# Kernel tuning notes

Hardware: AMD Instinct MI355X
Metric: run time of the kernel (lower is better)

Reference implementation:

```python
import jax, jax.numpy as jnp
import numpy as np

STATE_DIM = 28224  # 84*84*4 flattened Atari stack
N_EPISODE = 8192
FEATURE_DIM = 32
K_NEAREST = 10
C = 0.001
EPS_KERNEL = 0.001


def setup_inputs() -> dict:
    key = jax.random.key(0)
    ks = jax.random.split(key, 5)
    s = jax.random.normal(ks[0], (1, STATE_DIM), dtype=jnp.float32)
    episode = jax.random.normal(ks[1], (N_EPISODE, STATE_DIM), dtype=jnp.float32)
    dm2 = jnp.ones((1,), dtype=jnp.float32)  # running distance stat (torch inits 0.0; 1.0 avoids div-by-zero)
    # fan-in scaled weights so activations stay O(1)
    W1 = jax.random.normal(ks[2], (STATE_DIM, 128), dtype=jnp.float32) / np.sqrt(STATE_DIM)
    b1 = jnp.zeros((128,), dtype=jnp.float32)
    W2 = jax.random.normal(ks[3], (128, 64), dtype=jnp.float32) / np.sqrt(128.0)
    b2 = jnp.zeros((64,), dtype=jnp.float32)
    W3 = jax.random.normal(ks[4], (64, FEATURE_DIM), dtype=jnp.float32) / np.sqrt(64.0)
    b3 = jnp.zeros((FEATURE_DIM,), dtype=jnp.float32)
    return {"s": s, "episode": episode, "dm2": dm2,
            "W1": W1, "b1": b1, "W2": W2, "b2": b2, "W3": W3, "b3": b3}


def _embed(x, W1, b1, W2, b2, W3, b3):
    h = jax.nn.relu(x @ W1 + b1)
    h = jax.nn.relu(h @ W2 + b2)
    return h @ W3 + b3  # [*, FEATURE_DIM]


def reference(s, episode, dm2, W1, b1, W2, b2, W3, b3):
    z_s = _embed(s, W1, b1, W2, b2, W3, b3)          # [1, F]
    z_ep = _embed(episode, W1, b1, W2, b2, W3, b3)   # [N, F]
    dist = jnp.linalg.norm(z_s - z_ep, axis=1)       # [N]
    kernel = EPS_KERNEL / (dist / dm2[0] + EPS_KERNEL)
    top_k_kernel, _ = jax.lax.top_k(kernel, K_NEAREST)           # largest kernel values
    neg_top_dist, _ = jax.lax.top_k(-dist, K_NEAREST)            # smallest distances
    top_k_dist = -neg_top_dist
    new_dm2 = 0.99 * dm2[0] + 0.01 * jnp.mean(top_k_dist)        # running-stat update
    reward_episodic = 1.0 / (jnp.sqrt(jnp.mean(top_k_kernel)) + C)
    return reward_episodic, new_dm2
```

## Files before the change

### kernel.cpp

```cpp
#include <hip/hip_runtime.h>
#include <hip/hip_bf16.h>

typedef __attribute__((ext_vector_type(8))) __bf16 bf16x8;
typedef __attribute__((ext_vector_type(4))) float f32x4;
typedef __attribute__((ext_vector_type(4))) unsigned short u16x4;

#define STATE_DIM 28224
#define NEP 8192
#define MPAD 8320
#define KSPLIT 7
#define KSTEPS 63
#define BK 64
#define EPSK 0.001f
#define CC 0.001f

#define WT_BYTES   (441 * 8192 * 2)
#define PART_BYTES (KSPLIT * MPAD * 128 * 4)
#define Z_BYTES    (MPAD * 32 * 4)
#define DIST_BYTES (NEP * 4)
#define WS_NEEDED  (WT_BYTES + PART_BYTES + Z_BYTES + DIST_BYTES)

__device__ __forceinline__ unsigned short f2bf(float f) {
    unsigned int u = __float_as_uint(f);
    u += 0x7fffu + ((u >> 16) & 1u);
    return (unsigned short)(u >> 16);
}

__device__ __forceinline__ void glds16(const void* g, void* l) {
    __builtin_amdgcn_global_load_lds(
        (const __attribute__((address_space(1))) unsigned int*)g,
        (__attribute__((address_space(3))) unsigned int*)l, 16, 0, 0);
}

__global__ __launch_bounds__(256) void prep_wt(const float* __restrict__ W1,
                                               unsigned short* __restrict__ WtS) {
    __shared__ __align__(16) unsigned short img[8192];
    const int c = blockIdx.x;
    const int tid = threadIdx.x;
    const int k0 = c * 64;
#pragma unroll
    for (int i = 0; i < 32; ++i) {
        const int f = i * 256 + tid;
        const int k = f >> 7, n = f & 127;
        const float wv = W1[(size_t)(k0 + k) * 128 + n];
        const int ad = ((n * 128 + k * 2) ^ ((n & 7) << 4)) >> 1;
        img[ad] = f2bf(wv);
    }
    __syncthreads();
    unsigned short* dst = WtS + (size_t)c * 8192;
#pragma unroll
    for (int i = 0; i < 4; ++i) {
        const int f = i * 256 + tid;
        *reinterpret_cast<uint4*>(dst + f * 8) =
            *reinterpret_cast<const uint4*>(img + f * 8);
    }
}

__global__ __launch_bounds__(256, 2) void gemm1(const float* __restrict__ ep,
                                                const float* __restrict__ s,
                                                const unsigned short* __restrict__ WtS,
                                                float* __restrict__ part) {
    __shared__ __align__(16) unsigned char smA[128 * 64 * 2];
    __shared__ __align__(16) unsigned char smB[2][128 * 64 * 2];

    const int bid = blockIdx.x;
    const int ks = bid / 65;
    const int mt = bid % 65;
    const int tid = threadIdx.x;
    const int kBase = ks * (KSTEPS * BK);
    const int chunkBase = ks * KSTEPS;

    const int mBase = tid >> 4;
    const int kOff = (tid & 15) * 4;
    const int swzW = (mBase & 7) << 4;

    const bool last = (mt == 64);
    const int rowBase = mt * 128;

    float4 aR[8];

    auto loadA = [&](int kc) {
#pragma unroll
        for (int i = 0; i < 8; ++i) {
            const int m = mBase + i * 16;
            const int rg = rowBase + m;
            if (!last) {
                aR[i] = *reinterpret_cast<const float4*>(ep + (size_t)rg * STATE_DIM + kc + kOff);
            } else {
                if (rg < NEP)
                    aR[i] = *reinterpret_cast<const float4*>(ep + (size_t)rg * STATE_DIM + kc + kOff);
                else if (rg == NEP)
                    aR[i] = *reinterpret_cast<const float4*>(s + kc + kOff);
                else
                    aR[i] = make_float4(0.f, 0.f, 0.f, 0.f);
            }
        }
    };

    const int w = tid >> 6;
    const int lane = tid & 63;

    auto stageB = [&](int chunkIdx, int buf) {
        const char* cb = (const char*)(WtS + (size_t)chunkIdx * 8192);
#pragma unroll
        for (int r2 = 0; r2 < 4; ++r2) {
            const int off = ((r2 << 2) + w) << 10;
            glds16(cb + off + (lane << 4), &smB[buf][off]);
        }
    };

    auto writeLdsA = [&]() {
#pragma unroll
        for (int i = 0; i < 8; ++i) {
            const int m = mBase + i * 16;
            u16x4 av;
            av[0] = f2bf(aR[i].x); av[1] = f2bf(aR[i].y);
            av[2] = f2bf(aR[i].z); av[3] = f2bf(aR[i].w);
            const int ad = (m * 128 + kOff * 2) ^ swzW;
            *reinterpret_cast<u16x4*>(smA + ad) = av;
        }
    };

    const int wr = w >> 1, wc = w & 1;
    const int l15 = lane & 15, lq = lane >> 4;
    const int swzF = (l15 & 7) << 4;

    f32x4 acc[4][4] = {};

    auto compute = [&](int buf) {
#pragma unroll
        for (int kh = 0; kh < 2; ++kh) {
            bf16x8 af[4], bf[4];
#pragma unroll
            for (int mf = 0; mf < 4; ++mf) {
                const int row = wr * 64 + mf * 16 + l15;
                const int ad = (row * 128 + (kh * 32 + lq * 8) * 2) ^ swzF;
                af[mf] = *reinterpret_cast<const bf16x8*>(smA + ad);
            }
#pragma unroll
            for (int nf = 0; nf < 4; ++nf) {
                const int row = wc * 64 + nf * 16 + l15;
                const int ad = (row * 128 + (kh * 32 + lq * 8) * 2) ^ swzF;
                bf[nf] = *reinterpret_cast<const bf16x8*>(smB[buf] + ad);
            }
#pragma unroll
            for (int mf = 0; mf < 4; ++mf)
#pragma unroll
                for (int nf = 0; nf < 4; ++nf)
                    acc[mf][nf] = __builtin_amdgcn_mfma_f32_16x16x32_bf16(
                        af[mf], bf[nf], acc[mf][nf], 0, 0, 0);
        }
    };

    loadA(kBase);
    stageB(chunkBase, 0);
    int buf = 0;
    for (int t2 = 0; t2 < KSTEPS; ++t2) {
        __syncthreads();
        writeLdsA();
        __syncthreads();
        if (t2 + 1 < KSTEPS) {
            loadA(kBase + (t2 + 1) * BK);
            stageB(chunkBase + t2 + 1, buf ^ 1);
        }
        compute(buf);
        buf ^= 1;
    }

    float* po = part + ((size_t)ks * MPAD + rowBase) * 128;
#pragma unroll
    for (int mf = 0; mf < 4; ++mf)
#pragma unroll
        for (int nf = 0; nf < 4; ++nf)
#pragma unroll
            for (int v = 0; v < 4; ++v) {
                const int row = wr * 64 + mf * 16 + lq * 4 + v;
                const int col = wc * 64 + nf * 16 + l15;
                po[(size_t)row * 128 + col] = acc[mf][nf][v];
            }
}

__global__ __launch_bounds__(256) void mlp23(const float* __restrict__ part,
                                             const float* __restrict__ b1,
                                             const float* __restrict__ W2,
                                             const float* __restrict__ b2,
                                             const float* __restrict__ W3,
                                             const float* __restrict__ b3,
                                             float* __restrict__ z) {
    __shared__ float W2t[64 * 129];
    __shared__ float W3t[32 * 65];
    __shared__ float b1L[128], b2L[64], b3L[32];
    __shared__ float h1buf[4][128];
    __shared__ float h2buf[4][64];

    const int tid = threadIdx.x;
#pragma unroll
    for (int i = 0; i < 32; ++i) {
        int f = tid + i * 256;
        W2t[(f & 63) * 129 + (f >> 6)] = W2[f];
    }
#pragma unroll
    for (int i = 0; i < 8; ++i) {
        int f = tid + i * 256;
        W3t[(f & 31) * 65 + (f >> 5)] = W3[f];
    }
    if (tid < 128) b1L[tid] = b1[tid];
    if (tid < 64) b2L[tid] = b2[tid];
    if (tid < 32) b3L[tid] = b3[tid];
    __syncthreads();

    const int w = tid >> 6, l = tid & 63;
    const int base = blockIdx.x * 16 + w * 4;
    for (int rr = 0; rr < 4; ++rr) {
        const int r = base + rr;
        if (r > NEP) continue;
        float h1a = b1L[l], h1b = b1L[l + 64];
#pragma unroll
        for (int p = 0; p < KSPLIT; ++p) {
            const float* pp = part + ((size_t)p * MPAD + r) * 128;
            h1a += pp[l];
            h1b += pp[l + 64];
        }
        h1a = fmaxf(h1a, 0.f);
        h1b = fmaxf(h1b, 0.f);
        h1buf[w][l] = h1a;
        h1buf[w][l + 64] = h1b;
        float a2 = b2L[l];
#pragma unroll 8
        for (int k = 0; k < 128; ++k) a2 += h1buf[w][k] * W2t[l * 129 + k];
        a2 = fmaxf(a2, 0.f);
        h2buf[w][l] = a2;
        const int c = l & 31;
        float a3 = b3L[c];
#pragma unroll 8
        for (int k = 0; k < 64; ++k) a3 += h2buf[w][k] * W3t[c * 65 + k];
        if (l < 32) z[(size_t)r * 32 + c] = a3;
    }
}

__global__ __launch_bounds__(256) void dist_k(const float* __restrict__ z,
                                              float* __restrict__ dist) {
    __shared__ float zs[32];
    const int t = threadIdx.x;
    if (t < 32) zs[t] = z[(size_t)NEP * 32 + t];
    __syncthreads();
    const int r = blockIdx.x * 256 + t;
    const float* zr = z + (size_t)r * 32;
    float d2 = 0.f;
#pragma unroll
    for (int c2 = 0; c2 < 32; ++c2) {
        const float d = zr[c2] - zs[c2];
        d2 += d * d;
    }
    dist[r] = sqrtf(d2);
}

__global__ __launch_bounds__(256) void top10_k(const float* __restrict__ dist,
                                               const float* __restrict__ dm2,
                                               float* __restrict__ out) {
    const int t = threadIdx.x;
    float v[32];
#pragma unroll
    for (int i = 0; i < 32; ++i) v[i] = dist[i * 256 + t];

    __shared__ float wv[4];
    __shared__ int wi[4];

    const float dm = dm2[0];
    float sd = 0.f, sk = 0.f;

    for (int round = 0; round < 10; ++round) {
        float bv = 3.0e38f;
        int bi = 0x7fffffff;
#pragma unroll
        for (int i = 0; i < 32; ++i) {
            const float x = v[i];
            const int idx = i * 256 + t;
            if (x < bv) { bv = x; bi = idx; }
        }
#pragma unroll
        for (int sft = 1; sft < 64; sft <<= 1) {
            const float ov = __shfl_xor(bv, sft);
            const int oi = __shfl_xor(bi, sft);
            if (ov < bv || (ov == bv && oi < bi)) { bv = ov; bi = oi; }
        }
        const int wid = t >> 6;
        if ((t & 63) == 0) { wv[wid] = bv; wi[wid] = bi; }
        __syncthreads();
        bv = wv[0]; bi = wi[0];
#pragma unroll
        for (int k = 1; k < 4; ++k) {
            const float ov = wv[k]; const int oi = wi[k];
            if (ov < bv || (ov == bv && oi < bi)) { bv = ov; bi = oi; }
        }
        __syncthreads();
#pragma unroll
        for (int i = 0; i < 32; ++i)
            if (bi == i * 256 + t) v[i] = 3.0e38f;
        sd += bv;
        sk += EPSK / (bv / dm + EPSK);
    }

    if (t == 0) {
        const float meand = sd * 0.1f;
        const float meank = sk * 0.1f;
        out[0] = 1.0f / (sqrtf(meank) + CC);
        out[1] = 0.99f * dm + 0.01f * meand;
    }
}

extern "C" void kernel_launch(void* const* d_in, const int* in_sizes, int n_in,
                              void* d_out, int out_size, void* d_ws, size_t ws_size,
                              hipStream_t stream) {
    const float* s   = (const float*)d_in[0];
    const float* ep  = (const float*)d_in[1];
    const float* dm2 = (const float*)d_in[2];
    const float* W1  = (const float*)d_in[3];
    const float* b1  = (const float*)d_in[4];
    const float* W2  = (const float*)d_in[5];
    const float* b2  = (const float*)d_in[6];
    const float* W3  = (const float*)d_in[7];
    const float* b3  = (const float*)d_in[8];
    float* out = (float*)d_out;

    if (ws_size < (size_t)WS_NEEDED) return;

    unsigned short* WtS = (unsigned short*)d_ws;
    float* part = (float*)((char*)d_ws + WT_BYTES);
    float* zbuf = (float*)((char*)d_ws + WT_BYTES + PART_BYTES);
    float* dist = (float*)((char*)d_ws + WT_BYTES + PART_BYTES + Z_BYTES);

    hipLaunchKernelGGL(prep_wt, dim3(441), dim3(256), 0, stream, W1, WtS);
    hipLaunchKernelGGL(gemm1, dim3(65 * KSPLIT), dim3(256), 0, stream, ep, s, WtS, part);
    hipLaunchKernelGGL(mlp23, dim3(520), dim3(256), 0, stream, part, b1, W2, b2, W3, b3, zbuf);
    hipLaunchKernelGGL(dist_k, dim3(32), dim3(256), 0, stream, zbuf, dist);
    hipLaunchKernelGGL(top10_k, dim3(1), dim3(256), 0, stream, dist, dm2, out);
}
```

Baseline: 228.5 us.

## Halve GEMM1 M-tile to 64 rows for more blocks and split MLP dot-product chains

The first-layer GEMM now uses 64-row M tiles instead of 128. That raises the grid from 455 to 903 blocks and shrinks per-block LDS and accumulator registers, so three blocks can fit per CU. Each thread now loads 4 contiguous float4 per row, and each wave covers all 64 rows across 32 output columns. The intent is better occupancy and CU coverage for what is a memory-bound streaming of the 924MB episode matrix. Separately, the layer-2/3 dot products in mlp23 use several independent accumulators to break serial FMA dependencies, at the cost of a changed floating-point summation order.

Result: slower. 273.2 us (+19.5%).

```diff
diff --git a/kernel.cpp b/kernel.cpp
--- a/kernel.cpp
+++ b/kernel.cpp
@@ -7,7 +7,8 @@
 
 #define STATE_DIM 28224
 #define NEP 8192
-#define MPAD 8320
+#define NMT 129
+#define MPAD 8256
 #define KSPLIT 7
 #define KSTEPS 63
 #define BK 64
@@ -56,45 +57,46 @@
     }
 }
 
-__global__ __launch_bounds__(256, 2) void gemm1(const float* __restrict__ ep,
+__global__ __launch_bounds__(256, 3) void gemm1(const float* __restrict__ ep,
                                                 const float* __restrict__ s,
                                                 const unsigned short* __restrict__ WtS,
                                                 float* __restrict__ part) {
-    __shared__ __align__(16) unsigned char smA[128 * 64 * 2];
+    __shared__ __align__(16) unsigned char smA[64 * 64 * 2];
     __shared__ __align__(16) unsigned char smB[2][128 * 64 * 2];
 
     const int bid = blockIdx.x;
-    const int ks = bid / 65;
-    const int mt = bid % 65;
+    const int ks = bid / NMT;
+    const int mt = bid % NMT;
     const int tid = threadIdx.x;
     const int kBase = ks * (KSTEPS * BK);
     const int chunkBase = ks * KSTEPS;
 
-    const int mBase = tid >> 4;
-    const int kOff = (tid & 15) * 4;
-    const int swzW = (mBase & 7) << 4;
-
-    const bool last = (mt == 64);
-    const int rowBase = mt * 128;
-
-    float4 aR[8];
+    const int mRow = tid >> 2;
+    const int kSeg = (tid & 3) * 16;
+    const int swzW = (mRow & 7) << 4;
+
+    const bool last = (mt == NMT - 1);
+    const int rowBase = mt * 64;
+
+    float4 aR[4];
 
     auto loadA = [&](int kc) {
-#pragma unroll
-        for (int i = 0; i < 8; ++i) {
-            const int m = mBase + i * 16;
-            const int rg = rowBase + m;
-            if (!last) {
-                aR[i] = *reinterpret_cast<const float4*>(ep + (size_t)rg * STATE_DIM + kc + kOff);
-            } else {
-                if (rg < NEP)
-                    aR[i] = *reinterpret_cast<const float4*>(ep + (size_t)rg * STATE_DIM + kc + kOff);
-                else if (rg == NEP)
-                    aR[i] = *reinterpret_cast<const float4*>(s + kc + kOff);
-                else
-                    aR[i] = make_float4(0.f, 0.f, 0.f, 0.f);
-            }
-        }
+        const int rg = rowBase + mRow;
+        const float* src;
+        if (!last) {
+            src = ep + (size_t)rg * STATE_DIM + kc + kSeg;
+        } else if (rg < NEP) {
+            src = ep + (size_t)rg * STATE_DIM + kc + kSeg;
+        } else if (rg == NEP) {
+            src = s + kc + kSeg;
+        } else {
+#pragma unroll
+            for (int j = 0; j < 4; ++j) aR[j] = make_float4(0.f, 0.f, 0.f, 0.f);
+            return;
+        }
+#pragma unroll
+        for (int j = 0; j < 4; ++j)
+            aR[j] = *reinterpret_cast<const float4*>(src + j * 4);
     };
 
     const int w = tid >> 6;
@@ -111,42 +113,40 @@
 
     auto writeLdsA = [&]() {
 #pragma unroll
-        for (int i = 0; i < 8; ++i) {
-            const int m = mBase + i * 16;
+        for (int j = 0; j < 4; ++j) {
             u16x4 av;
-            av[0] = f2bf(aR[i].x); av[1] = f2bf(aR[i].y);
-            av[2] = f2bf(aR[i].z); av[3] = f2bf(aR[i].w);
-            const int ad = (m * 128 + kOff * 2) ^ swzW;
+            av[0] = f2bf(aR[j].x); av[1] = f2bf(aR[j].y);
+            av[2] = f2bf(aR[j].z); av[3] = f2bf(aR[j].w);
+            const int ad = (mRow * 128 + (kSeg + j * 4) * 2) ^ swzW;
             *reinterpret_cast<u16x4*>(smA + ad) = av;
         }
     };
 
-    const int wr = w >> 1, wc = w & 1;
     const int l15 = lane & 15, lq = lane >> 4;
     const int swzF = (l15 & 7) << 4;
 
-    f32x4 acc[4][4] = {};
+    f32x4 acc[4][2] = {};
 
     auto compute = [&](int buf) {
 #pragma unroll
         for (int kh = 0; kh < 2; ++kh) {
-            bf16x8 af[4], bf[4];
+            bf16x8 af[4], bf[2];
 #pragma unroll
             for (int mf = 0; mf < 4; ++mf) {
-                const int row = wr * 64 + mf * 16 + l15;
+                const int row = mf * 16 + l15;
                 const int ad = (row * 128 + (kh * 32 + lq * 8) * 2) ^ swzF;
                 af[mf] = *reinterpret_cast<const bf16x8*>(smA + ad);
             }
 #pragma unroll
-            for (int nf = 0; nf < 4; ++nf) {
-                const int row = wc * 64 + nf * 16 + l15;
+            for (int nf = 0; nf < 2; ++nf) {
+                const int row = w * 32 + nf * 16 + l15;
                 const int ad = (row * 128 + (kh * 32 + lq * 8) * 2) ^ swzF;
                 bf[nf] = *reinterpret_cast<const bf16x8*>(smB[buf] + ad);
             }
 #pragma unroll
             for (int mf = 0; mf < 4; ++mf)
 #pragma unroll
-                for (int nf = 0; nf < 4; ++nf)
+                for (int nf = 0; nf < 2; ++nf)
                     acc[mf][nf] = __builtin_amdgcn_mfma_f32_16x16x32_bf16(
                         af[mf], bf[nf], acc[mf][nf], 0, 0, 0);
         }
@@ -171,11 +171,11 @@
 #pragma unroll
     for (int mf = 0; mf < 4; ++mf)
 #pragma unroll
-        for (int nf = 0; nf < 4; ++nf)
+        for (int nf = 0; nf < 2; ++nf)
 #pragma unroll
             for (int v = 0; v < 4; ++v) {
-                const int row = wr * 64 + mf * 16 + lq * 4 + v;
-                const int col = wc * 64 + nf * 16 + l15;
+                const int row = mf * 16 + lq * 4 + v;
+                const int col = w * 32 + nf * 16 + l15;
                 po[(size_t)row * 128 + col] = acc[mf][nf][v];
             }
 }
@@ -225,16 +225,28 @@
         h1b = fmaxf(h1b, 0.f);
         h1buf[w][l] = h1a;
         h1buf[w][l + 64] = h1b;
-        float a2 = b2L[l];
+        float s0 = 0.f, s1 = 0.f, s2 = 0.f, s3 = 0.f;
+        const float* wr2 = &W2t[l * 129];
+        const float* hb = h1buf[w];
 #pragma unroll 8
-        for (int k = 0; k < 128; ++k) a2 += h1buf[w][k] * W2t[l * 129 + k];
-        a2 = fmaxf(a2, 0.f);
+        for (int k = 0; k < 32; ++k) {
+            s0 += hb[k]      * wr2[k];
+            s1 += hb[k + 32] * wr2[k + 32];
+            s2 += hb[k + 64] * wr2[k + 64];
+            s3 += hb[k + 96] * wr2[k + 96];
+        }
+        float a2 = fmaxf(b2L[l] + ((s0 + s1) + (s2 + s3)), 0.f);
         h2buf[w][l] = a2;
         const int c = l & 31;
-        float a3 = b3L[c];
+        const float* wr3 = &W3t[c * 65];
+        const float* h2 = h2buf[w];
+        float t0 = 0.f, t1 = 0.f;
 #pragma unroll 8
-        for (int k = 0; k < 64; ++k) a3 += h2buf[w][k] * W3t[c * 65 + k];
-        if (l < 32) z[(size_t)r * 32 + c] = a3;
+        for (int k = 0; k < 32; ++k) {
+            t0 += h2[k]      * wr3[k];
+            t1 += h2[k + 32] * wr3[k + 32];
+        }
+        if (l < 32) z[(size_t)r * 32 + c] = b3L[c] + t0 + t1;
     }
 }
 
@@ -331,8 +343,8 @@
     float* dist = (float*)((char*)d_ws + WT_BYTES + PART_BYTES + Z_BYTES);
 
     hipLaunchKernelGGL(prep_wt, dim3(441), dim3(256), 0, stream, W1, WtS);
-    hipLaunchKernelGGL(gemm1, dim3(65 * KSPLIT), dim3(256), 0, stream, ep, s, WtS, part);
-    hipLaunchKernelGGL(mlp23, dim3(520), dim3(256), 0, stream, part, b1, W2, b2, W3, b3, zbuf);
+    hipLaunchKernelGGL(gemm1, dim3(NMT * KSPLIT), dim3(256), 0, stream, ep, s, WtS, part);
+    hipLaunchKernelGGL(mlp23, dim3(MPAD / 16), dim3(256), 0, stream, part, b1, W2, b2, W3, b3, zbuf);
     hipLaunchKernelGGL(dist_k, dim3(32), dim3(256), 0, stream, zbuf, dist);
     hipLaunchKernelGGL(top10_k, dim3(1), dim3(256), 0, stream, dist, dm2, out);
 }
```

## Load GEMM operands directly into registers, dropping LDS staging and block barriers

Applied to the files above, without the earlier changes.

The first-layer GEMM no longer stages A and B tiles through shared memory. Each lane now loads its MFMA fragments straight from global memory into registers, using double-buffered register sets and an occasional s_barrier to keep waves loosely in step. W1 is pre-transposed into a plain row-major [128 x STATE_DIM] bf16 layout to suit this. The last M-tile reuses the s row and writes only row 0. The mlp23 dot products are split into several independent partial sums. The change removes LDS traffic and __syncthreads, but each fragment load is a strided 32-byte access per lane, so global coalescing and cache reuse across waves may suffer.

Result: slower. 413.1 us (+80.8%).

```diff
diff --git a/kernel.cpp b/kernel.cpp
--- a/kernel.cpp
+++ b/kernel.cpp
@@ -3,18 +3,17 @@
 
 typedef __attribute__((ext_vector_type(8))) __bf16 bf16x8;
 typedef __attribute__((ext_vector_type(4))) float f32x4;
-typedef __attribute__((ext_vector_type(4))) unsigned short u16x4;
 
 #define STATE_DIM 28224
 #define NEP 8192
 #define MPAD 8320
 #define KSPLIT 7
-#define KSTEPS 63
-#define BK 64
+#define KRANGE 4032
+#define KSTEPS 126
 #define EPSK 0.001f
 #define CC 0.001f
 
-#define WT_BYTES   (441 * 8192 * 2)
+#define WT_BYTES   (128 * 28224 * 2)
 #define PART_BYTES (KSPLIT * MPAD * 128 * 4)
 #define Z_BYTES    (MPAD * 32 * 4)
 #define DIST_BYTES (NEP * 4)
@@ -26,148 +25,100 @@
     return (unsigned short)(u >> 16);
 }
 
-__device__ __forceinline__ void glds16(const void* g, void* l) {
-    __builtin_amdgcn_global_load_lds(
-        (const __attribute__((address_space(1))) unsigned int*)g,
-        (__attribute__((address_space(3))) unsigned int*)l, 16, 0, 0);
-}
-
 __global__ __launch_bounds__(256) void prep_wt(const float* __restrict__ W1,
-                                               unsigned short* __restrict__ WtS) {
-    __shared__ __align__(16) unsigned short img[8192];
-    const int c = blockIdx.x;
-    const int tid = threadIdx.x;
-    const int k0 = c * 64;
-#pragma unroll
-    for (int i = 0; i < 32; ++i) {
-        const int f = i * 256 + tid;
-        const int k = f >> 7, n = f & 127;
-        const float wv = W1[(size_t)(k0 + k) * 128 + n];
-        const int ad = ((n * 128 + k * 2) ^ ((n & 7) << 4)) >> 1;
-        img[ad] = f2bf(wv);
+                                               unsigned short* __restrict__ Wt) {
+    __shared__ float tile[32 * 65];
+    const int b = blockIdx.x;
+    const int kt = b % 441, nt = b / 441;
+    const int k0 = kt * 64, n0 = nt * 32;
+    const int t = threadIdx.x;
+#pragma unroll
+    for (int i = 0; i < 8; ++i) {
+        int f = t + i * 256;
+        int kk = f >> 5, nn = f & 31;
+        tile[nn * 65 + kk] = W1[(size_t)(k0 + kk) * 128 + n0 + nn];
     }
     __syncthreads();
-    unsigned short* dst = WtS + (size_t)c * 8192;
-#pragma unroll
-    for (int i = 0; i < 4; ++i) {
-        const int f = i * 256 + tid;
-        *reinterpret_cast<uint4*>(dst + f * 8) =
-            *reinterpret_cast<const uint4*>(img + f * 8);
+#pragma unroll
+    for (int i = 0; i < 8; ++i) {
+        int f = t + i * 256;
+        int nn = f >> 6, kk = f & 63;
+        Wt[(size_t)(n0 + nn) * STATE_DIM + k0 + kk] = f2bf(tile[nn * 65 + kk]);
     }
 }
 
 __global__ __launch_bounds__(256, 2) void gemm1(const float* __restrict__ ep,
                                                 const float* __restrict__ s,
-                                                const unsigned short* __restrict__ WtS,
+                                                const unsigned short* __restrict__ Wt,
                                                 float* __restrict__ part) {
-    __shared__ __align__(16) unsigned char smA[128 * 64 * 2];
-    __shared__ __align__(16) unsigned char smB[2][128 * 64 * 2];
-
     const int bid = blockIdx.x;
     const int ks = bid / 65;
     const int mt = bid % 65;
     const int tid = threadIdx.x;
-    const int kBase = ks * (KSTEPS * BK);
-    const int chunkBase = ks * KSTEPS;
-
-    const int mBase = tid >> 4;
-    const int kOff = (tid & 15) * 4;
-    const int swzW = (mBase & 7) << 4;
-
-    const bool last = (mt == 64);
-    const int rowBase = mt * 128;
-
-    float4 aR[8];
-
-    auto loadA = [&](int kc) {
-#pragma unroll
-        for (int i = 0; i < 8; ++i) {
-            const int m = mBase + i * 16;
-            const int rg = rowBase + m;
-            if (!last) {
-                aR[i] = *reinterpret_cast<const float4*>(ep + (size_t)rg * STATE_DIM + kc + kOff);
-            } else {
-                if (rg < NEP)
-                    aR[i] = *reinterpret_cast<const float4*>(ep + (size_t)rg * STATE_DIM + kc + kOff);
-                else if (rg == NEP)
-                    aR[i] = *reinterpret_cast<const float4*>(s + kc + kOff);
-                else
-                    aR[i] = make_float4(0.f, 0.f, 0.f, 0.f);
-            }
-        }
-    };
-
-    const int w = tid >> 6;
-    const int lane = tid & 63;
-
-    auto stageB = [&](int chunkIdx, int buf) {
-        const char* cb = (const char*)(WtS + (size_t)chunkIdx * 8192);
-#pragma unroll
-        for (int r2 = 0; r2 < 4; ++r2) {
-            const int off = ((r2 << 2) + w) << 10;
-            glds16(cb + off + (lane << 4), &smB[buf][off]);
-        }
-    };
-
-    auto writeLdsA = [&]() {
-#pragma unroll
-        for (int i = 0; i < 8; ++i) {
-            const int m = mBase + i * 16;
-            u16x4 av;
-            av[0] = f2bf(aR[i].x); av[1] = f2bf(aR[i].y);
-            av[2] = f2bf(aR[i].z); av[3] = f2bf(aR[i].w);
-            const int ad = (m * 128 + kOff * 2) ^ swzW;
-            *reinterpret_cast<u16x4*>(smA + ad) = av;
-        }
-    };
-
+    const int w = tid >> 6, lane = tid & 63;
     const int wr = w >> 1, wc = w & 1;
     const int l15 = lane & 15, lq = lane >> 4;
-    const int swzF = (l15 & 7) << 4;
+    const int kBase = ks * KRANGE;
+    const bool last = (mt == 64);
+
+    const float* aP[4];
+    const unsigned short* bP[4];
+#pragma unroll
+    for (int mf = 0; mf < 4; ++mf) {
+        const int row = mt * 128 + wr * 64 + mf * 16 + l15;
+        aP[mf] = last ? (s + kBase + lq * 8)
+                      : (ep + (size_t)row * STATE_DIM + kBase + lq * 8);
+    }
+#pragma unroll
+    for (int nf = 0; nf < 4; ++nf) {
+        const int n = wc * 64 + nf * 16 + l15;
+        bP[nf] = Wt + (size_t)n * STATE_DIM + kBase + lq * 8;
+    }
 
     f32x4 acc[4][4] = {};
 
-    auto compute = [&](int buf) {
-#pragma unroll
-        for (int kh = 0; kh < 2; ++kh) {
-            bf16x8 af[4], bf[4];
-#pragma unroll
-            for (int mf = 0; mf < 4; ++mf) {
-                const int row = wr * 64 + mf * 16 + l15;
-                const int ad = (row * 128 + (kh * 32 + lq * 8) * 2) ^ swzF;
-                af[mf] = *reinterpret_cast<const bf16x8*>(smA + ad);
-            }
-#pragma unroll
-            for (int nf = 0; nf < 4; ++nf) {
-                const int row = wc * 64 + nf * 16 + l15;
-                const int ad = (row * 128 + (kh * 32 + lq * 8) * 2) ^ swzF;
-                bf[nf] = *reinterpret_cast<const bf16x8*>(smB[buf] + ad);
-            }
-#pragma unroll
-            for (int mf = 0; mf < 4; ++mf)
-#pragma unroll
-                for (int nf = 0; nf < 4; ++nf)
-                    acc[mf][nf] = __builtin_amdgcn_mfma_f32_16x16x32_bf16(
-                        af[mf], bf[nf], acc[mf][nf], 0, 0, 0);
-        }
-    };
-
-    loadA(kBase);
-    stageB(chunkBase, 0);
-    int buf = 0;
-    for (int t2 = 0; t2 < KSTEPS; ++t2) {
-        __syncthreads();
-        writeLdsA();
-        __syncthreads();
-        if (t2 + 1 < KSTEPS) {
-            loadA(kBase + (t2 + 1) * BK);
-            stageB(chunkBase + t2 + 1, buf ^ 1);
-        }
-        compute(buf);
-        buf ^= 1;
-    }
-
-    float* po = part + ((size_t)ks * MPAD + rowBase) * 128;
+    float4 a0A[4], a1A[4], a0B[4], a1B[4];
+    uint4 bA[4], bB[4];
+
+#define LOADS(A0, A1, BB, t2)                                                   \
+    {                                                                           \
+        const int ko = (t2) * 32;                                               \
+        _Pragma("unroll") for (int mf = 0; mf < 4; ++mf) {                      \
+            A0[mf] = *reinterpret_cast<const float4*>(aP[mf] + ko);             \
+            A1[mf] = *reinterpret_cast<const float4*>(aP[mf] + ko + 4);         \
+        }                                                                       \
+        _Pragma("unroll") for (int nf = 0; nf < 4; ++nf)                        \
+            BB[nf] = *reinterpret_cast<const uint4*>(bP[nf] + ko);              \
+    }
+
+#define COMPUTE(A0, A1, BB)                                                     \
+    {                                                                           \
+        bf16x8 af[4];                                                           \
+        _Pragma("unroll") for (int mf = 0; mf < 4; ++mf) {                      \
+            af[mf][0] = (__bf16)A0[mf].x; af[mf][1] = (__bf16)A0[mf].y;         \
+            af[mf][2] = (__bf16)A0[mf].z; af[mf][3] = (__bf16)A0[mf].w;         \
+            af[mf][4] = (__bf16)A1[mf].x; af[mf][5] = (__bf16)A1[mf].y;         \
+            af[mf][6] = (__bf16)A1[mf].z; af[mf][7] = (__bf16)A1[mf].w;         \
+        }                                                                       \
+        _Pragma("unroll") for (int mf = 0; mf < 4; ++mf)                        \
+            _Pragma("unroll") for (int nf = 0; nf < 4; ++nf)                    \
+                acc[mf][nf] = __builtin_amdgcn_mfma_f32_16x16x32_bf16(          \
+                    af[mf], *reinterpret_cast<const bf16x8*>(&BB[nf]),          \
+                    acc[mf][nf], 0, 0, 0);                                      \
+    }
+
+    LOADS(a0A, a1A, bA, 0);
+    for (int t2 = 0; t2 < KSTEPS; t2 += 2) {
+        LOADS(a0B, a1B, bB, t2 + 1);
+        COMPUTE(a0A, a1A, bA);
+        if (t2 + 2 < KSTEPS) LOADS(a0A, a1A, bA, t2 + 2);
+        COMPUTE(a0B, a1B, bB);
+        if ((t2 & 15) == 14) __builtin_amdgcn_s_barrier();
+    }
+#undef LOADS
+#undef COMPUTE
+
+    float* po = part + ((size_t)ks * MPAD + mt * 128) * 128;
 #pragma unroll
     for (int mf = 0; mf < 4; ++mf)
 #pragma unroll
@@ -176,7 +127,8 @@
             for (int v = 0; v < 4; ++v) {
                 const int row = wr * 64 + mf * 16 + lq * 4 + v;
                 const int col = wc * 64 + nf * 16 + l15;
-                po[(size_t)row * 128 + col] = acc[mf][nf][v];
+                if (!last || row == 0)
+                    po[(size_t)row * 128 + col] = acc[mf][nf][v];
             }
 }
 
@@ -225,16 +177,28 @@
         h1b = fmaxf(h1b, 0.f);
         h1buf[w][l] = h1a;
         h1buf[w][l + 64] = h1b;
-        float a2 = b2L[l];
+        float s0 = 0.f, s1 = 0.f, s2 = 0.f, s3 = 0.f;
+        const float* wr2 = &W2t[l * 129];
+        const float* hb = h1buf[w];
 #pragma unroll 8
-        for (int k = 0; k < 128; ++k) a2 += h1buf[w][k] * W2t[l * 129 + k];
-        a2 = fmaxf(a2, 0.f);
+        for (int k = 0; k < 32; ++k) {
+            s0 += hb[k]      * wr2[k];
+            s1 += hb[k + 32] * wr2[k + 32];
+            s2 += hb[k + 64] * wr2[k + 64];
+            s3 += hb[k + 96] * wr2[k + 96];
+        }
+        float a2 = fmaxf(b2L[l] + ((s0 + s1) + (s2 + s3)), 0.f);
         h2buf[w][l] = a2;
         const int c = l & 31;
-        float a3 = b3L[c];
+        const float* wr3 = &W3t[c * 65];
+        const float* h2 = h2buf[w];
+        float t0 = 0.f, t1 = 0.f;
 #pragma unroll 8
-        for (int k = 0; k < 64; ++k) a3 += h2buf[w][k] * W3t[c * 65 + k];
-        if (l < 32) z[(size_t)r * 32 + c] = a3;
+        for (int k = 0; k < 32; ++k) {
+            t0 += h2[k]      * wr3[k];
+            t1 += h2[k + 32] * wr3[k + 32];
+        }
+        if (l < 32) z[(size_t)r * 32 + c] = b3L[c] + t0 + t1;
     }
 }
 
@@ -325,14 +289,14 @@
 
     if (ws_size < (size_t)WS_NEEDED) return;
 
-    unsigned short* WtS = (unsigned short*)d_ws;
+    unsigned short* Wt = (unsigned short*)d_ws;
     float* part = (float*)((char*)d_ws + WT_BYTES);
     float* zbuf = (float*)((char*)d_ws + WT_BYTES + PART_BYTES);
     float* dist = (float*)((char*)d_ws + WT_BYTES + PART_BYTES + Z_BYTES);
 
-    hipLaunchKernelGGL(prep_wt, dim3(441), dim3(256), 0, stream, W1, WtS);
-    hipLaunchKernelGGL(gemm1, dim3(65 * KSPLIT), dim3(256), 0, stream, ep, s, WtS, part);
-    hipLaunchKernelGGL(mlp23, dim3(520), dim3(256), 0, stream, part, b1, W2, b2, W3, b3, zbuf);
+    hipLaunchKernelGGL(prep_wt, dim3(441 * 4), dim3(256), 0, stream, W1, Wt);
+    hipLaunchKernelGGL(gemm1, dim3(65 * KSPLIT), dim3(256), 0, stream, ep, s, Wt, part);
+    hipLaunchKernelGGL(mlp23, dim3(MPAD / 16), dim3(256), 0, stream, part, b1, W2, b2, W3, b3, zbuf);
     hipLaunchKernelGGL(dist_k, dim3(32), dim3(256), 0, stream, zbuf, dist);
     hipLaunchKernelGGL(top10_k, dim3(1), dim3(256), 0, stream, dist, dm2, out);
 }
```

## Deepen gemm1 prefetch to two stages with triple-buffered B and manual waitcnt

Applied to the files above, without the earlier changes.

Moves gemm1 from a single-step prefetch to a two-step lookahead. A tiles are held in two register sets and B tiles are triple-buffered in shared memory, with explicit vmcnt/lgkmcnt waits and scheduling barriers in place of plain __syncthreads. The aim is to hide more of the global-memory latency when streaming the large episode matrix. The A-row pointers are precomputed so the last tile no longer branches on every load, and padding rows are zeroed at LDS write. The mlp23 dot products are split into several independent accumulators to shorten dependency chains. The cost is higher register and LDS use, which may lower occupancy, and the hand-counted vmcnt(12) must match the actual number of outstanding loads.

After: 259.4 us. 1.14x slower.

```diff
diff --git a/kernel.cpp b/kernel.cpp
--- a/kernel.cpp
+++ b/kernel.cpp
@@ -61,7 +61,7 @@
                                                 const unsigned short* __restrict__ WtS,
                                                 float* __restrict__ part) {
     __shared__ __align__(16) unsigned char smA[128 * 64 * 2];
-    __shared__ __align__(16) unsigned char smB[2][128 * 64 * 2];
+    __shared__ __align__(16) unsigned char smB[3][128 * 64 * 2];
 
     const int bid = blockIdx.x;
     const int ks = bid / 65;
@@ -77,46 +77,47 @@
     const bool last = (mt == 64);
     const int rowBase = mt * 128;
 
-    float4 aR[8];
-
-    auto loadA = [&](int kc) {
-#pragma unroll
-        for (int i = 0; i < 8; ++i) {
-            const int m = mBase + i * 16;
-            const int rg = rowBase + m;
-            if (!last) {
-                aR[i] = *reinterpret_cast<const float4*>(ep + (size_t)rg * STATE_DIM + kc + kOff);
-            } else {
-                if (rg < NEP)
-                    aR[i] = *reinterpret_cast<const float4*>(ep + (size_t)rg * STATE_DIM + kc + kOff);
-                else if (rg == NEP)
-                    aR[i] = *reinterpret_cast<const float4*>(s + kc + kOff);
-                else
-                    aR[i] = make_float4(0.f, 0.f, 0.f, 0.f);
-            }
-        }
-    };
-
     const int w = tid >> 6;
     const int lane = tid & 63;
 
-    auto stageB = [&](int chunkIdx, int buf) {
+    const float* aSrc[8];
+#pragma unroll
+    for (int i = 0; i < 8; ++i) {
+        const int rg = rowBase + mBase + i * 16;
+        if (!last)            aSrc[i] = ep + (size_t)rg * STATE_DIM;
+        else if (rg < NEP)    aSrc[i] = ep + (size_t)rg * STATE_DIM;
+        else                  aSrc[i] = s;
+    }
+
+    float4 Ra[8], Rb[8];
+
+    auto loadA = [&](float4* R, int kc) {
+#pragma unroll
+        for (int i = 0; i < 8; ++i)
+            R[i] = *reinterpret_cast<const float4*>(aSrc[i] + kc + kOff);
+    };
+
+    auto stageB = [&](int chunkIdx, unsigned char* bbuf) {
         const char* cb = (const char*)(WtS + (size_t)chunkIdx * 8192);
 #pragma unroll
         for (int r2 = 0; r2 < 4; ++r2) {
             const int off = ((r2 << 2) + w) << 10;
-            glds16(cb + off + (lane << 4), &smB[buf][off]);
+            glds16(cb + off + (lane << 4), bbuf + off);
         }
     };
 
-    auto writeLdsA = [&]() {
+    auto writeLdsA = [&](const float4* R) {
 #pragma unroll
         for (int i = 0; i < 8; ++i) {
-            const int m = mBase + i * 16;
+            float4 a = R[i];
+            if (last) {
+                const int rg = rowBase + mBase + i * 16;
+                if (rg > NEP) a = make_float4(0.f, 0.f, 0.f, 0.f);
+            }
             u16x4 av;
-            av[0] = f2bf(aR[i].x); av[1] = f2bf(aR[i].y);
-            av[2] = f2bf(aR[i].z); av[3] = f2bf(aR[i].w);
-            const int ad = (m * 128 + kOff * 2) ^ swzW;
+            av[0] = f2bf(a.x); av[1] = f2bf(a.y);
+            av[2] = f2bf(a.z); av[3] = f2bf(a.w);
+            const int ad = ((mBase + i * 16) * 128 + kOff * 2) ^ swzW;
             *reinterpret_cast<u16x4*>(smA + ad) = av;
         }
     };
@@ -127,7 +128,7 @@
 
     f32x4 acc[4][4] = {};
 
-    auto compute = [&](int buf) {
+    auto compute = [&](const unsigned char* bbuf) {
 #pragma unroll
         for (int kh = 0; kh < 2; ++kh) {
             bf16x8 af[4], bf[4];
@@ -141,7 +142,7 @@
             for (int nf = 0; nf < 4; ++nf) {
                 const int row = wc * 64 + nf * 16 + l15;
                 const int ad = (row * 128 + (kh * 32 + lq * 8) * 2) ^ swzF;
-                bf[nf] = *reinterpret_cast<const bf16x8*>(smB[buf] + ad);
+                bf[nf] = *reinterpret_cast<const bf16x8*>(bbuf + ad);
             }
 #pragma unroll
             for (int mf = 0; mf < 4; ++mf)
@@ -152,19 +153,32 @@
         }
     };
 
-    loadA(kBase);
-    stageB(chunkBase, 0);
-    int buf = 0;
+    loadA(Ra, kBase);
+    stageB(chunkBase, smB[0]);
+    loadA(Rb, kBase + BK);
+    stageB(chunkBase + 1, smB[1]);
+
+    int b0 = 0, b2 = 2;
     for (int t2 = 0; t2 < KSTEPS; ++t2) {
-        __syncthreads();
-        writeLdsA();
-        __syncthreads();
-        if (t2 + 1 < KSTEPS) {
-            loadA(kBase + (t2 + 1) * BK);
-            stageB(chunkBase + t2 + 1, buf ^ 1);
-        }
-        compute(buf);
-        buf ^= 1;
+        if (t2 + 1 < KSTEPS) { asm volatile("s_waitcnt vmcnt(12)" ::: "memory"); }
+        else                 { asm volatile("s_waitcnt vmcnt(0)"  ::: "memory"); }
+        __builtin_amdgcn_sched_barrier(0);
+        __builtin_amdgcn_s_barrier();
+        __builtin_amdgcn_sched_barrier(0);
+        if (t2 & 1) writeLdsA(Rb); else writeLdsA(Ra);
+        asm volatile("s_waitcnt lgkmcnt(0)" ::: "memory");
+        __builtin_amdgcn_sched_barrier(0);
+        __builtin_amdgcn_s_barrier();
+        __builtin_amdgcn_sched_barrier(0);
+        if (t2 + 2 < KSTEPS) {
+            if (t2 & 1) loadA(Rb, kBase + (t2 + 2) * BK);
+            else        loadA(Ra, kBase + (t2 + 2) * BK);
+            stageB(chunkBase + t2 + 2, smB[b2]);
+        }
+        __builtin_amdgcn_sched_barrier(0);
+        compute(smB[b0]);
+        b0 = (b0 == 2) ? 0 : b0 + 1;
+        b2 = (b2 == 2) ? 0 : b2 + 1;
     }
 
     float* po = part + ((size_t)ks * MPAD + rowBase) * 128;
@@ -225,16 +239,28 @@
         h1b = fmaxf(h1b, 0.f);
         h1buf[w][l] = h1a;
         h1buf[w][l + 64] = h1b;
-        float a2 = b2L[l];
+        float s0 = 0.f, s1 = 0.f, s2 = 0.f, s3 = 0.f;
+        const float* wr2 = &W2t[l * 129];
+        const float* hb = h1buf[w];
 #pragma unroll 8
-        for (int k = 0; k < 128; ++k) a2 += h1buf[w][k] * W2t[l * 129 + k];
-        a2 = fmaxf(a2, 0.f);
+        for (int k = 0; k < 32; ++k) {
+            s0 += hb[k]      * wr2[k];
+            s1 += hb[k + 32] * wr2[k + 32];
+            s2 += hb[k + 64] * wr2[k + 64];
+            s3 += hb[k + 96] * wr2[k + 96];
+        }
+        float a2 = fmaxf(b2L[l] + ((s0 + s1) + (s2 + s3)), 0.f);
         h2buf[w][l] = a2;
         const int c = l & 31;
-        float a3 = b3L[c];
+        const float* wr3 = &W3t[c * 65];
+        const float* h2 = h2buf[w];
+        float t0 = 0.f, t1 = 0.f;
 #pragma unroll 8
-        for (int k = 0; k < 64; ++k) a3 += h2buf[w][k] * W3t[c * 65 + k];
-        if (l < 32) z[(size_t)r * 32 + c] = a3;
+        for (int k = 0; k < 32; ++k) {
+            t0 += h2[k]      * wr3[k];
+            t1 += h2[k + 32] * wr3[k + 32];
+        }
+        if (l < 32) z[(size_t)r * 32 + c] = b3L[c] + t0 + t1;
     }
 }
 
@@ -332,7 +358,7 @@
 
     hipLaunchKernelGGL(prep_wt, dim3(441), dim3(256), 0, stream, W1, WtS);
     hipLaunchKernelGGL(gemm1, dim3(65 * KSPLIT), dim3(256), 0, stream, ep, s, WtS, part);
-    hipLaunchKernelGGL(mlp23, dim3(520), dim3(256), 0, stream, part, b1, W2, b2, W3, b3, zbuf);
+    hipLaunchKernelGGL(mlp23, dim3(MPAD / 16), dim3(256), 0, stream, part, b1, W2, b2, W3, b3, zbuf);
     hipLaunchKernelGGL(dist_k, dim3(32), dim3(256), 0, stream, zbuf, dist);
     hipLaunchKernelGGL(top10_k, dim3(1), dim3(256), 0, stream, dist, dm2, out);
 }
```
